# Kernel optimization log

Hardware: AMD Instinct MI355X
Metric: run time of the kernel (lower is better)

Reference implementation:

```python
import jax, jax.numpy as jnp
import numpy as np

NUM_HEADS = 16
D_KV = 64
NUM_BUCKETS = 32
MAX_DISTANCE = 128


def _relative_position_bucket(rel_pos, num_buckets=NUM_BUCKETS, max_distance=MAX_DISTANCE):
    # bidirectional bucketing (dec_or_not=False -> b_di=True in source)
    nb = num_buckets // 2
    buckets = (rel_pos > 0).astype(jnp.int32) * nb
    rel = jnp.abs(rel_pos)
    max_exact = nb // 2
    is_small = rel < max_exact
    # guard log(0); masked out by is_small anyway
    rel_if_large = max_exact + (
        jnp.log(jnp.maximum(rel, 1).astype(jnp.float32) / max_exact)
        / np.log(max_distance / max_exact) * (nb - max_exact)
    ).astype(jnp.int32)
    rel_if_large = jnp.minimum(rel_if_large, nb - 1)
    return buckets + jnp.where(is_small, rel, rel_if_large)


def setup_inputs() -> dict:
    key = jax.random.key(0)
    ks = jax.random.split(key, 6)
    B, S, D = 2, 2048, 1024
    s = 1.0 / np.sqrt(D)
    return {
        "hidden_states": jax.random.normal(ks[0], (B, S, D), jnp.float32),
        "Wq": jax.random.normal(ks[1], (D, NUM_HEADS * D_KV), jnp.float32) * s,
        "Wk": jax.random.normal(ks[2], (D, NUM_HEADS * D_KV), jnp.float32) * s,
        "Wv": jax.random.normal(ks[3], (D, NUM_HEADS * D_KV), jnp.float32) * s,
        "Wo": jax.random.normal(ks[4], (NUM_HEADS * D_KV, D), jnp.float32) * s,
        "rel_emb": jax.random.normal(ks[5], (NUM_BUCKETS, NUM_HEADS), jnp.float32),
    }


def reference(hidden_states, Wq, Wk, Wv, Wo, rel_emb):
    B, S, D = hidden_states.shape
    H, Dh = NUM_HEADS, D_KV

    def heads(x):  # [B,S,H*Dh] -> [B,H,S,Dh]
        return x.reshape(B, S, H, Dh).transpose(0, 2, 1, 3)

    q = heads(hidden_states @ Wq)
    k = heads(hidden_states @ Wk)
    v = heads(hidden_states @ Wv)

    # T5 attention: no 1/sqrt(d) scaling
    scores = jnp.einsum("bhqd,bhkd->bhqk", q, k)

    # relative position bias (bias_cal)
    pos = jnp.arange(S)
    rel_pos = pos[None, :] - pos[:, None]  # [S_q, S_k]
    buckets = _relative_position_bucket(rel_pos)
    bias = rel_emb[buckets]                       # [S,S,H]
    bias = bias.transpose(2, 0, 1)[None]          # [1,H,S,S]

    scores = scores + bias
    attn = jax.nn.softmax(scores.astype(jnp.float32), axis=-1).astype(scores.dtype)
    # dropout p=0 in eval -> identity
    out = jnp.einsum("bhqk,bhkd->bhqd", attn, v)
    out = out.transpose(0, 2, 1, 3).reshape(B, S, H * Dh)
    return out @ Wo
```

## Files before the change

kernel.cpp:

```cpp
#include <hip/hip_runtime.h>

typedef __bf16 bf16x8 __attribute__((ext_vector_type(8)));
typedef float f32x4 __attribute__((ext_vector_type(4)));

#define LDK 72
#define LOG2E 1.44269504088896f

__device__ __forceinline__ unsigned short bfbits(float x) {
  __bf16 h = (__bf16)x;
  return __builtin_bit_cast(unsigned short, h);
}

__global__ void bias_table_kernel(const float* __restrict__ rel_emb,
                                  float* __restrict__ tab) {
  int i = blockIdx.x * 256 + threadIdx.x;
  int h = i >> 12;
  int idx = i & 4095;
  int rp = idx - 2048;
  int base = (rp > 0) ? 16 : 0;
  int rel = rp < 0 ? -rp : rp;
  int b;
  if (rel < 8) {
    b = rel;
  } else {
    b = 8 + (int)(log2f((float)rel * 0.125f) * 2.0f);
    if (b > 15) b = 15;
  }
  tab[h * 4096 + idx] = rel_emb[(base + b) * 16 + h] * LOG2E;
}

__global__ __launch_bounds__(256)
void transpose_w_kernel(const float* __restrict__ W0, const float* __restrict__ W1,
                        const float* __restrict__ W2, const float* __restrict__ W3,
                        unsigned short* __restrict__ T0, unsigned short* __restrict__ T1,
                        unsigned short* __restrict__ T2, unsigned short* __restrict__ T3) {
  __shared__ __align__(16) unsigned short Tlds[64 * 68];
  const int mz = blockIdx.z;
  const float* W = mz == 0 ? W0 : (mz == 1 ? W1 : (mz == 2 ? W2 : W3));
  unsigned short* T = mz == 0 ? T0 : (mz == 1 ? T1 : (mz == 2 ? T2 : T3));
  const int k0 = blockIdx.y * 64, n0 = blockIdx.x * 64, tid = threadIdx.x;
#pragma unroll
  for (int p = 0; p < 4; ++p) {
    int idx = p * 256 + tid;
    int kk = idx >> 4, nc = idx & 15;
    float4 v = *(const float4*)(W + (size_t)(k0 + kk) * 1024 + n0 + nc * 4);
    ushort4 s;
    s.x = bfbits(v.x); s.y = bfbits(v.y); s.z = bfbits(v.z); s.w = bfbits(v.w);
    *(ushort4*)(Tlds + kk * 68 + nc * 4) = s;
  }
  __syncthreads();
#pragma unroll
  for (int p = 0; p < 2; ++p) {
    int idx = p * 256 + tid;
    int n = idx >> 3, c = idx & 7;
    unsigned short tmp[8];
#pragma unroll
    for (int j = 0; j < 8; ++j) tmp[j] = Tlds[(c * 8 + j) * 68 + n];
    *(uint4*)(T + (size_t)(n0 + n) * 1024 + k0 + c * 8) = *(const uint4*)tmp;
  }
}

template <bool A_F32, bool OUT_F32, int BN>
__global__ __launch_bounds__(256)
void gemm_kernel(const void* __restrict__ Av,
                 const unsigned short* __restrict__ Wt0,
                 const unsigned short* __restrict__ Wt1,
                 const unsigned short* __restrict__ Wt2,
                 void* __restrict__ O0v, void* __restrict__ O1v, void* __restrict__ O2v,
                 float scale0) {
  constexpr int NBLK = 1024 / BN;
  constexpr int NT = BN / 32;
  __shared__ __align__(16) unsigned short Alds[128 * LDK];
  __shared__ __align__(16) unsigned short Wlds[BN * LDK];
  const int tid = threadIdx.x;
  const int which = blockIdx.x / NBLK;
  const int n0 = (blockIdx.x % NBLK) * BN;
  const int m0 = blockIdx.y * 128;
  const unsigned short* Wt = which == 0 ? Wt0 : (which == 1 ? Wt1 : Wt2);
  void* Ov = which == 0 ? O0v : (which == 1 ? O1v : O2v);
  const int wave = tid >> 6, lane = tid & 63, quad = lane >> 4, col = lane & 15;
  const int wm = (wave >> 1) * 64, wn = (wave & 1) * (BN / 2);

  f32x4 acc[4][NT] = {};

  for (int kt = 0; kt < 16; ++kt) {
    const int k0 = kt * 64;
    __syncthreads();
    if (A_F32) {
      const float* A = (const float*)Av;
#pragma unroll
      for (int p = 0; p < 8; ++p) {
        int idx = p * 256 + tid;
        int m = idx >> 4, c = idx & 15;
        float4 v = *(const float4*)(A + (size_t)(m0 + m) * 1024 + k0 + c * 4);
        ushort4 s;
        s.x = bfbits(v.x); s.y = bfbits(v.y); s.z = bfbits(v.z); s.w = bfbits(v.w);
        *(ushort4*)(Alds + m * LDK + c * 4) = s;
      }
    } else {
      const unsigned short* A = (const unsigned short*)Av;
#pragma unroll
      for (int p = 0; p < 4; ++p) {
        int idx = p * 256 + tid;
        int m = idx >> 3, c = idx & 7;
        uint4 v = *(const uint4*)(A + (size_t)(m0 + m) * 1024 + k0 + c * 8);
        *(uint4*)(Alds + m * LDK + c * 8) = v;
      }
    }
#pragma unroll
    for (int p = 0; p < BN / 32; ++p) {
      int idx = p * 256 + tid;
      int n = idx >> 3, c = idx & 7;
      uint4 v = *(const uint4*)(Wt + (size_t)(n0 + n) * 1024 + k0 + c * 8);
      *(uint4*)(Wlds + n * LDK + c * 8) = v;
    }
    __syncthreads();
#pragma unroll
    for (int ks = 0; ks < 2; ++ks) {
      bf16x8 af[4], wf[NT];
#pragma unroll
      for (int mt = 0; mt < 4; ++mt)
        af[mt] = *(const bf16x8*)(Alds + (wm + mt * 16 + col) * LDK + ks * 32 + quad * 8);
#pragma unroll
      for (int nt = 0; nt < NT; ++nt)
        wf[nt] = *(const bf16x8*)(Wlds + (wn + nt * 16 + col) * LDK + ks * 32 + quad * 8);
#pragma unroll
      for (int mt = 0; mt < 4; ++mt)
#pragma unroll
        for (int nt = 0; nt < NT; ++nt)
          acc[mt][nt] = __builtin_amdgcn_mfma_f32_16x16x32_bf16(af[mt], wf[nt], acc[mt][nt], 0, 0, 0);
    }
  }
  if (!OUT_F32 && which == 2) {
    unsigned short* Ot = (unsigned short*)Ov;
#pragma unroll
    for (int nt = 0; nt < NT; ++nt)
#pragma unroll
      for (int mt = 0; mt < 4; ++mt) {
        int n = n0 + wn + nt * 16 + col;
        int m = m0 + wm + mt * 16 + quad * 4;
        ushort4 s;
        s.x = bfbits(acc[mt][nt][0]); s.y = bfbits(acc[mt][nt][1]);
        s.z = bfbits(acc[mt][nt][2]); s.w = bfbits(acc[mt][nt][3]);
        *(ushort4*)(Ot + (size_t)n * 4096 + m) = s;
      }
  } else {
    const float sc = (which == 0) ? scale0 : 1.0f;
#pragma unroll
    for (int mt = 0; mt < 4; ++mt)
#pragma unroll
      for (int nt = 0; nt < NT; ++nt)
#pragma unroll
        for (int r = 0; r < 4; ++r) {
          int m = m0 + wm + mt * 16 + quad * 4 + r;
          int n = n0 + wn + nt * 16 + col;
          float x = acc[mt][nt][r] * sc;
          if (OUT_F32)
            ((float*)Ov)[(size_t)m * 1024 + n] = x;
          else
            ((unsigned short*)Ov)[(size_t)m * 1024 + n] = bfbits(x);
        }
  }
}

__global__ __launch_bounds__(256)
void attn_kernel(unsigned short* __restrict__ q_ws,
                 const unsigned short* __restrict__ k_ws,
                 const unsigned short* __restrict__ vt_ws,
                 const float* __restrict__ bias_tab) {
  __shared__ __align__(16) unsigned short Klds[64 * LDK];
  __shared__ __align__(16) unsigned short Vlds[64 * LDK];
  __shared__ __align__(16) unsigned short Plds[128 * LDK];
  __shared__ float bias_lds[192];
  __shared__ float l_sh[128];
  const int tid = threadIdx.x;
  const int q0 = blockIdx.x * 128;
  const int bh = blockIdx.y;
  const int b = bh >> 4, h = bh & 15;
  const int wave = tid >> 6, lane = tid & 63, quad = lane >> 4, col = lane & 15;

  bf16x8 qf[2][2];
#pragma unroll
  for (int nt = 0; nt < 2; ++nt) {
    size_t row = (size_t)(b * 2048 + q0 + wave * 32 + nt * 16 + col) * 1024 + h * 64;
    qf[nt][0] = *(const bf16x8*)(q_ws + row + quad * 8);
    qf[nt][1] = *(const bf16x8*)(q_ws + row + 32 + quad * 8);
  }

  float l_lane[2] = {0.f, 0.f};
  f32x4 of[2][4] = {};

  for (int kt = 0; kt < 32; ++kt) {
    const int k0 = kt * 64;
    __syncthreads();
#pragma unroll
    for (int p = 0; p < 2; ++p) {
      int idx = p * 256 + tid;
      int key = idx >> 3, c = idx & 7;
      *(uint4*)(Klds + key * LDK + c * 8) =
          *(const uint4*)(k_ws + (size_t)(b * 2048 + k0 + key) * 1024 + h * 64 + c * 8);
    }
#pragma unroll
    for (int p = 0; p < 2; ++p) {
      int idx = p * 256 + tid;
      int d = idx >> 3, c = idx & 7;
      *(uint4*)(Vlds + d * LDK + c * 8) =
          *(const uint4*)(vt_ws + (size_t)(h * 64 + d) * 4096 + b * 2048 + k0 + c * 8);
    }
    if (tid < 191) bias_lds[tid] = bias_tab[h * 4096 + 2048 + k0 - q0 - 127 + tid];
    __syncthreads();

    f32x4 st[4][2];
#pragma unroll
    for (int mt = 0; mt < 4; ++mt)
#pragma unroll
      for (int nt = 0; nt < 2; ++nt)
#pragma unroll
        for (int r = 0; r < 4; ++r)
          st[mt][nt][r] =
              bias_lds[(mt * 16 + quad * 4 + r) - (wave * 32 + nt * 16 + col) + 127];
#pragma unroll
    for (int ks = 0; ks < 2; ++ks)
#pragma unroll
      for (int mt = 0; mt < 4; ++mt) {
        bf16x8 kf = *(const bf16x8*)(Klds + (mt * 16 + col) * LDK + ks * 32 + quad * 8);
        st[mt][0] = __builtin_amdgcn_mfma_f32_16x16x32_bf16(kf, qf[0][ks], st[mt][0], 0, 0, 0);
        st[mt][1] = __builtin_amdgcn_mfma_f32_16x16x32_bf16(kf, qf[1][ks], st[mt][1], 0, 0, 0);
      }

#pragma unroll
    for (int nt = 0; nt < 2; ++nt)
#pragma unroll
      for (int mt = 0; mt < 4; ++mt) {
        float p0 = __builtin_amdgcn_exp2f(st[mt][nt][0] - 64.f);
        float p1 = __builtin_amdgcn_exp2f(st[mt][nt][1] - 64.f);
        float p2 = __builtin_amdgcn_exp2f(st[mt][nt][2] - 64.f);
        float p3 = __builtin_amdgcn_exp2f(st[mt][nt][3] - 64.f);
        l_lane[nt] += (p0 + p1) + (p2 + p3);
        ushort4 pk;
        pk.x = bfbits(p0); pk.y = bfbits(p1); pk.z = bfbits(p2); pk.w = bfbits(p3);
        *(ushort4*)(Plds + (wave * 32 + nt * 16 + col) * LDK + mt * 16 + quad * 4) = pk;
      }
    __threadfence_block();

#pragma unroll
    for (int ks = 0; ks < 2; ++ks) {
      bf16x8 pf0 = *(const bf16x8*)(Plds + (wave * 32 + col) * LDK + ks * 32 + quad * 8);
      bf16x8 pf1 = *(const bf16x8*)(Plds + (wave * 32 + 16 + col) * LDK + ks * 32 + quad * 8);
#pragma unroll
      for (int dn = 0; dn < 4; ++dn) {
        bf16x8 vf = *(const bf16x8*)(Vlds + (dn * 16 + col) * LDK + ks * 32 + quad * 8);
        of[0][dn] = __builtin_amdgcn_mfma_f32_16x16x32_bf16(pf0, vf, of[0][dn], 0, 0, 0);
        of[1][dn] = __builtin_amdgcn_mfma_f32_16x16x32_bf16(pf1, vf, of[1][dn], 0, 0, 0);
      }
    }
  }

#pragma unroll
  for (int nt = 0; nt < 2; ++nt) {
    l_lane[nt] += __shfl_xor(l_lane[nt], 16, 64);
    l_lane[nt] += __shfl_xor(l_lane[nt], 32, 64);
  }
  l_sh[wave * 32 + col] = l_lane[0];
  l_sh[wave * 32 + 16 + col] = l_lane[1];
  __syncthreads();
#pragma unroll
  for (int mtp = 0; mtp < 2; ++mtp)
#pragma unroll
    for (int r = 0; r < 4; ++r) {
      float inv = 1.0f / fmaxf(l_sh[wave * 32 + mtp * 16 + quad * 4 + r], 1e-30f);
      size_t row = (size_t)(b * 2048 + q0 + wave * 32 + mtp * 16 + quad * 4 + r);
#pragma unroll
      for (int dn = 0; dn < 4; ++dn)
        q_ws[row * 1024 + h * 64 + dn * 16 + col] = bfbits(of[mtp][dn][r] * inv);
    }
}

extern "C" void kernel_launch(void* const* d_in, const int* in_sizes, int n_in,
                              void* d_out, int out_size, void* d_ws, size_t ws_size,
                              hipStream_t stream) {
  const float* hidden = (const float*)d_in[0];
  const float* Wq = (const float*)d_in[1];
  const float* Wk = (const float*)d_in[2];
  const float* Wv = (const float*)d_in[3];
  const float* Wo = (const float*)d_in[4];
  const float* rel_emb = (const float*)d_in[5];
  float* out = (float*)d_out;

  unsigned short* q_ws = (unsigned short*)d_ws;
  unsigned short* k_ws = q_ws + 4194304;
  unsigned short* vt_ws = k_ws + 4194304;
  unsigned short* wt_q = vt_ws + 4194304;
  unsigned short* wt_k = wt_q + 1048576;
  unsigned short* wt_v = wt_k + 1048576;
  unsigned short* wt_o = wt_v + 1048576;
  float* bias_tab = (float*)(wt_o + 1048576);

  bias_table_kernel<<<256, 256, 0, stream>>>(rel_emb, bias_tab);
  transpose_w_kernel<<<dim3(16, 16, 4), 256, 0, stream>>>(
      Wq, Wk, Wv, Wo, wt_q, wt_k, wt_v, wt_o);
  gemm_kernel<true, false, 128><<<dim3(24, 32), 256, 0, stream>>>(
      hidden, wt_q, wt_k, wt_v, q_ws, k_ws, vt_ws, LOG2E);
  attn_kernel<<<dim3(16, 32), 256, 0, stream>>>(q_ws, k_ws, vt_ws, bias_tab);
  gemm_kernel<false, true, 64><<<dim3(16, 32), 256, 0, stream>>>(
      q_ws, wt_o, wt_o, wt_o, out, out, out, 1.0f);
}
```

Before: 239.4 us.

## Split attention over key halves with merge pass; pre-convert hidden states to bf16

The attention kernel now splits the key range into two halves along a new grid dimension, doubling the block count from 512 to 1024 so more CUs are occupied. Each half writes unnormalized partial outputs and row sums to scratch, and a separate merge kernel adds them and normalizes. The merge is correct without max rescaling because the original kernel does not track a running max. Hidden states are also converted to bf16 once in a standalone kernel, so the QKV GEMM loads bf16 A tiles instead of converting fp32 in every block. The cost is extra global traffic for the partial outputs, two extra launches, and the partial sums being rounded to bf16.

```diff
diff --git a/kernel.cpp b/kernel.cpp
--- a/kernel.cpp
+++ b/kernel.cpp
@@ -30,6 +30,16 @@
 }
 
 __global__ __launch_bounds__(256)
+void hid_convert_kernel(const float* __restrict__ src, unsigned short* __restrict__ dst) {
+  int idx = (blockIdx.x * 256 + threadIdx.x) * 8;
+  float4 v0 = *(const float4*)(src + idx);
+  float4 v1 = *(const float4*)(src + idx + 4);
+  unsigned short o[8] = {bfbits(v0.x), bfbits(v0.y), bfbits(v0.z), bfbits(v0.w),
+                         bfbits(v1.x), bfbits(v1.y), bfbits(v1.z), bfbits(v1.w)};
+  *(uint4*)(dst + idx) = *(const uint4*)o;
+}
+
+__global__ __launch_bounds__(256)
 void transpose_w_kernel(const float* __restrict__ W0, const float* __restrict__ W1,
                         const float* __restrict__ W2, const float* __restrict__ W3,
                         unsigned short* __restrict__ T0, unsigned short* __restrict__ T1,
@@ -60,9 +70,9 @@
   }
 }
 
-template <bool A_F32, bool OUT_F32, int BN>
-__global__ __launch_bounds__(256)
-void gemm_kernel(const void* __restrict__ Av,
+template <bool OUT_F32, int BN>
+__global__ __launch_bounds__(256)
+void gemm_kernel(const unsigned short* __restrict__ A,
                  const unsigned short* __restrict__ Wt0,
                  const unsigned short* __restrict__ Wt1,
                  const unsigned short* __restrict__ Wt2,
@@ -86,26 +96,12 @@
   for (int kt = 0; kt < 16; ++kt) {
     const int k0 = kt * 64;
     __syncthreads();
-    if (A_F32) {
-      const float* A = (const float*)Av;
-#pragma unroll
-      for (int p = 0; p < 8; ++p) {
-        int idx = p * 256 + tid;
-        int m = idx >> 4, c = idx & 15;
-        float4 v = *(const float4*)(A + (size_t)(m0 + m) * 1024 + k0 + c * 4);
-        ushort4 s;
-        s.x = bfbits(v.x); s.y = bfbits(v.y); s.z = bfbits(v.z); s.w = bfbits(v.w);
-        *(ushort4*)(Alds + m * LDK + c * 4) = s;
-      }
-    } else {
-      const unsigned short* A = (const unsigned short*)Av;
-#pragma unroll
-      for (int p = 0; p < 4; ++p) {
-        int idx = p * 256 + tid;
-        int m = idx >> 3, c = idx & 7;
-        uint4 v = *(const uint4*)(A + (size_t)(m0 + m) * 1024 + k0 + c * 8);
-        *(uint4*)(Alds + m * LDK + c * 8) = v;
-      }
+#pragma unroll
+    for (int p = 0; p < 4; ++p) {
+      int idx = p * 256 + tid;
+      int m = idx >> 3, c = idx & 7;
+      uint4 v = *(const uint4*)(A + (size_t)(m0 + m) * 1024 + k0 + c * 8);
+      *(uint4*)(Alds + m * LDK + c * 8) = v;
     }
 #pragma unroll
     for (int p = 0; p < BN / 32; ++p) {
@@ -164,19 +160,21 @@
 }
 
 __global__ __launch_bounds__(256)
-void attn_kernel(unsigned short* __restrict__ q_ws,
+void attn_kernel(const unsigned short* __restrict__ q_ws,
                  const unsigned short* __restrict__ k_ws,
                  const unsigned short* __restrict__ vt_ws,
-                 const float* __restrict__ bias_tab) {
+                 const float* __restrict__ bias_tab,
+                 unsigned short* __restrict__ pO,
+                 float* __restrict__ l_ws) {
   __shared__ __align__(16) unsigned short Klds[64 * LDK];
   __shared__ __align__(16) unsigned short Vlds[64 * LDK];
   __shared__ __align__(16) unsigned short Plds[128 * LDK];
   __shared__ float bias_lds[192];
-  __shared__ float l_sh[128];
   const int tid = threadIdx.x;
   const int q0 = blockIdx.x * 128;
   const int bh = blockIdx.y;
   const int b = bh >> 4, h = bh & 15;
+  const int split = blockIdx.z;
   const int wave = tid >> 6, lane = tid & 63, quad = lane >> 4, col = lane & 15;
 
   bf16x8 qf[2][2];
@@ -190,7 +188,7 @@
   float l_lane[2] = {0.f, 0.f};
   f32x4 of[2][4] = {};
 
-  for (int kt = 0; kt < 32; ++kt) {
+  for (int kt = split * 16; kt < split * 16 + 16; ++kt) {
     const int k0 = kt * 64;
     __syncthreads();
 #pragma unroll
@@ -256,24 +254,43 @@
     }
   }
 
+  unsigned short* pOs = pO + (size_t)split * 4194304;
 #pragma unroll
   for (int nt = 0; nt < 2; ++nt) {
     l_lane[nt] += __shfl_xor(l_lane[nt], 16, 64);
     l_lane[nt] += __shfl_xor(l_lane[nt], 32, 64);
-  }
-  l_sh[wave * 32 + col] = l_lane[0];
-  l_sh[wave * 32 + 16 + col] = l_lane[1];
-  __syncthreads();
+    if (quad == 0)
+      l_ws[(size_t)split * 65536 + (b * 2048 + q0 + wave * 32 + nt * 16 + col) * 16 + h] =
+          l_lane[nt];
+  }
 #pragma unroll
   for (int mtp = 0; mtp < 2; ++mtp)
 #pragma unroll
     for (int r = 0; r < 4; ++r) {
-      float inv = 1.0f / fmaxf(l_sh[wave * 32 + mtp * 16 + quad * 4 + r], 1e-30f);
       size_t row = (size_t)(b * 2048 + q0 + wave * 32 + mtp * 16 + quad * 4 + r);
 #pragma unroll
       for (int dn = 0; dn < 4; ++dn)
-        q_ws[row * 1024 + h * 64 + dn * 16 + col] = bfbits(of[mtp][dn][r] * inv);
-    }
+        pOs[row * 1024 + h * 64 + dn * 16 + col] = bfbits(of[mtp][dn][r]);
+    }
+}
+
+__global__ __launch_bounds__(256)
+void merge_kernel(const unsigned short* __restrict__ pO,
+                  const float* __restrict__ l_ws,
+                  unsigned short* __restrict__ q_ws) {
+  int idx = (blockIdx.x * 256 + threadIdx.x) * 8;
+  int token = idx >> 10;
+  int h = (idx & 1023) >> 6;
+  float l0 = l_ws[token * 16 + h];
+  float l1 = l_ws[65536 + token * 16 + h];
+  float inv = 1.0f / fmaxf(l0 + l1, 1e-35f);
+  bf16x8 a = *(const bf16x8*)(pO + idx);
+  bf16x8 c = *(const bf16x8*)(pO + 4194304 + idx);
+  unsigned short o[8];
+#pragma unroll
+  for (int j = 0; j < 8; ++j)
+    o[j] = bfbits(((float)a[j] + (float)c[j]) * inv);
+  *(uint4*)(q_ws + idx) = *(const uint4*)o;
 }
 
 extern "C" void kernel_launch(void* const* d_in, const int* in_sizes, int n_in,
@@ -295,13 +312,18 @@
   unsigned short* wt_v = wt_k + 1048576;
   unsigned short* wt_o = wt_v + 1048576;
   float* bias_tab = (float*)(wt_o + 1048576);
+  unsigned short* scratch = (unsigned short*)d_out;
+  float* l_ws = (float*)wt_q;
 
   bias_table_kernel<<<256, 256, 0, stream>>>(rel_emb, bias_tab);
+  hid_convert_kernel<<<2048, 256, 0, stream>>>(hidden, scratch);
   transpose_w_kernel<<<dim3(16, 16, 4), 256, 0, stream>>>(
       Wq, Wk, Wv, Wo, wt_q, wt_k, wt_v, wt_o);
-  gemm_kernel<true, false, 128><<<dim3(24, 32), 256, 0, stream>>>(
-      hidden, wt_q, wt_k, wt_v, q_ws, k_ws, vt_ws, LOG2E);
-  attn_kernel<<<dim3(16, 32), 256, 0, stream>>>(q_ws, k_ws, vt_ws, bias_tab);
-  gemm_kernel<false, true, 64><<<dim3(16, 32), 256, 0, stream>>>(
+  gemm_kernel<false, 128><<<dim3(24, 32), 256, 0, stream>>>(
+      scratch, wt_q, wt_k, wt_v, q_ws, k_ws, vt_ws, LOG2E);
+  attn_kernel<<<dim3(16, 32, 2), 256, 0, stream>>>(
+      q_ws, k_ws, vt_ws, bias_tab, scratch, l_ws);
+  merge_kernel<<<2048, 256, 0, stream>>>(scratch, l_ws, q_ws);
+  gemm_kernel<true, 64><<<dim3(16, 32), 256, 0, stream>>>(
       q_ws, wt_o, wt_o, wt_o, out, out, out, 1.0f);
 }
```

Result: slower. 244.7 us (+2.2%).

## Use direct global-to-LDS loads in GEMM, pre-convert hidden to bf16, constant far bias

Applied to the files above, without the earlier changes.

Adds a kernel that converts hidden states to bf16 once, using the output buffer as scratch. The GEMM becomes bf16-only and stages tiles with global_load_lds straight into unpadded shared memory, removing register round-trips. The attention kernel treats key tiles beyond the max distance as a constant bias and skips the per-tile bias load. Risks include LDS bank conflicts from the removed padding and an extra kernel launch.

```diff
diff --git a/kernel.cpp b/kernel.cpp
--- a/kernel.cpp
+++ b/kernel.cpp
@@ -9,6 +9,12 @@
 __device__ __forceinline__ unsigned short bfbits(float x) {
   __bf16 h = (__bf16)x;
   return __builtin_bit_cast(unsigned short, h);
+}
+
+__device__ __forceinline__ void gload_lds16(const unsigned short* g, unsigned short* l) {
+  __builtin_amdgcn_global_load_lds(
+      (const __attribute__((address_space(1))) unsigned int*)(const void*)g,
+      (__attribute__((address_space(3))) unsigned int*)(void*)l, 16, 0, 0);
 }
 
 __global__ void bias_table_kernel(const float* __restrict__ rel_emb,
@@ -30,6 +36,16 @@
 }
 
 __global__ __launch_bounds__(256)
+void hid_convert_kernel(const float* __restrict__ src, unsigned short* __restrict__ dst) {
+  int idx = (blockIdx.x * 256 + threadIdx.x) * 8;
+  float4 v0 = *(const float4*)(src + idx);
+  float4 v1 = *(const float4*)(src + idx + 4);
+  unsigned short o[8] = {bfbits(v0.x), bfbits(v0.y), bfbits(v0.z), bfbits(v0.w),
+                         bfbits(v1.x), bfbits(v1.y), bfbits(v1.z), bfbits(v1.w)};
+  *(uint4*)(dst + idx) = *(const uint4*)o;
+}
+
+__global__ __launch_bounds__(256)
 void transpose_w_kernel(const float* __restrict__ W0, const float* __restrict__ W1,
                         const float* __restrict__ W2, const float* __restrict__ W3,
                         unsigned short* __restrict__ T0, unsigned short* __restrict__ T1,
@@ -60,9 +76,9 @@
   }
 }
 
-template <bool A_F32, bool OUT_F32, int BN>
+template <bool OUT_F32, int BN>
 __global__ __launch_bounds__(256)
-void gemm_kernel(const void* __restrict__ Av,
+void gemm_kernel(const unsigned short* __restrict__ A,
                  const unsigned short* __restrict__ Wt0,
                  const unsigned short* __restrict__ Wt1,
                  const unsigned short* __restrict__ Wt2,
@@ -70,8 +86,8 @@
                  float scale0) {
   constexpr int NBLK = 1024 / BN;
   constexpr int NT = BN / 32;
-  __shared__ __align__(16) unsigned short Alds[128 * LDK];
-  __shared__ __align__(16) unsigned short Wlds[BN * LDK];
+  __shared__ __align__(16) unsigned short Alds[128 * 64];
+  __shared__ __align__(16) unsigned short Wlds[BN * 64];
   const int tid = threadIdx.x;
   const int which = blockIdx.x / NBLK;
   const int n0 = (blockIdx.x % NBLK) * BN;
@@ -80,39 +96,26 @@
   void* Ov = which == 0 ? O0v : (which == 1 ? O1v : O2v);
   const int wave = tid >> 6, lane = tid & 63, quad = lane >> 4, col = lane & 15;
   const int wm = (wave >> 1) * 64, wn = (wave & 1) * (BN / 2);
+  const int wbase = tid & ~63;
 
   f32x4 acc[4][NT] = {};
 
   for (int kt = 0; kt < 16; ++kt) {
     const int k0 = kt * 64;
     __syncthreads();
-    if (A_F32) {
-      const float* A = (const float*)Av;
-#pragma unroll
-      for (int p = 0; p < 8; ++p) {
-        int idx = p * 256 + tid;
-        int m = idx >> 4, c = idx & 15;
-        float4 v = *(const float4*)(A + (size_t)(m0 + m) * 1024 + k0 + c * 4);
-        ushort4 s;
-        s.x = bfbits(v.x); s.y = bfbits(v.y); s.z = bfbits(v.z); s.w = bfbits(v.w);
-        *(ushort4*)(Alds + m * LDK + c * 4) = s;
-      }
-    } else {
-      const unsigned short* A = (const unsigned short*)Av;
-#pragma unroll
-      for (int p = 0; p < 4; ++p) {
-        int idx = p * 256 + tid;
-        int m = idx >> 3, c = idx & 7;
-        uint4 v = *(const uint4*)(A + (size_t)(m0 + m) * 1024 + k0 + c * 8);
-        *(uint4*)(Alds + m * LDK + c * 8) = v;
-      }
+#pragma unroll
+    for (int p = 0; p < 4; ++p) {
+      int idx = p * 256 + tid;
+      int m = idx >> 3, c = idx & 7;
+      gload_lds16(A + (size_t)(m0 + m) * 1024 + k0 + c * 8,
+                  Alds + (size_t)(p * 256 + wbase) * 8);
     }
 #pragma unroll
     for (int p = 0; p < BN / 32; ++p) {
       int idx = p * 256 + tid;
       int n = idx >> 3, c = idx & 7;
-      uint4 v = *(const uint4*)(Wt + (size_t)(n0 + n) * 1024 + k0 + c * 8);
-      *(uint4*)(Wlds + n * LDK + c * 8) = v;
+      gload_lds16(Wt + (size_t)(n0 + n) * 1024 + k0 + c * 8,
+                  Wlds + (size_t)(p * 256 + wbase) * 8);
     }
     __syncthreads();
 #pragma unroll
@@ -120,10 +123,10 @@
       bf16x8 af[4], wf[NT];
 #pragma unroll
       for (int mt = 0; mt < 4; ++mt)
-        af[mt] = *(const bf16x8*)(Alds + (wm + mt * 16 + col) * LDK + ks * 32 + quad * 8);
+        af[mt] = *(const bf16x8*)(Alds + (wm + mt * 16 + col) * 64 + ks * 32 + quad * 8);
 #pragma unroll
       for (int nt = 0; nt < NT; ++nt)
-        wf[nt] = *(const bf16x8*)(Wlds + (wn + nt * 16 + col) * LDK + ks * 32 + quad * 8);
+        wf[nt] = *(const bf16x8*)(Wlds + (wn + nt * 16 + col) * 64 + ks * 32 + quad * 8);
 #pragma unroll
       for (int mt = 0; mt < 4; ++mt)
 #pragma unroll
@@ -186,12 +189,16 @@
     qf[nt][0] = *(const bf16x8*)(q_ws + row + quad * 8);
     qf[nt][1] = *(const bf16x8*)(q_ws + row + 32 + quad * 8);
   }
+  const float bias_far_pos = bias_tab[h * 4096 + 2048 + 512];
+  const float bias_far_neg = bias_tab[h * 4096 + 2048 - 512];
 
   float l_lane[2] = {0.f, 0.f};
   f32x4 of[2][4] = {};
 
   for (int kt = 0; kt < 32; ++kt) {
     const int k0 = kt * 64;
+    const int diff = k0 - q0;
+    const bool far = (diff >= 256) || (diff <= -192);
     __syncthreads();
 #pragma unroll
     for (int p = 0; p < 2; ++p) {
@@ -207,18 +214,29 @@
       *(uint4*)(Vlds + d * LDK + c * 8) =
           *(const uint4*)(vt_ws + (size_t)(h * 64 + d) * 4096 + b * 2048 + k0 + c * 8);
     }
-    if (tid < 191) bias_lds[tid] = bias_tab[h * 4096 + 2048 + k0 - q0 - 127 + tid];
+    if (!far && tid < 191)
+      bias_lds[tid] = bias_tab[h * 4096 + 2048 + k0 - q0 - 127 + tid];
     __syncthreads();
 
     f32x4 st[4][2];
-#pragma unroll
-    for (int mt = 0; mt < 4; ++mt)
-#pragma unroll
-      for (int nt = 0; nt < 2; ++nt)
-#pragma unroll
-        for (int r = 0; r < 4; ++r)
-          st[mt][nt][r] =
-              bias_lds[(mt * 16 + quad * 4 + r) - (wave * 32 + nt * 16 + col) + 127];
+    if (far) {
+      const float c0 = (diff > 0) ? bias_far_pos : bias_far_neg;
+#pragma unroll
+      for (int mt = 0; mt < 4; ++mt)
+#pragma unroll
+        for (int nt = 0; nt < 2; ++nt)
+#pragma unroll
+          for (int r = 0; r < 4; ++r) st[mt][nt][r] = c0;
+    } else {
+#pragma unroll
+      for (int mt = 0; mt < 4; ++mt)
+#pragma unroll
+        for (int nt = 0; nt < 2; ++nt)
+#pragma unroll
+          for (int r = 0; r < 4; ++r)
+            st[mt][nt][r] =
+                bias_lds[(mt * 16 + quad * 4 + r) - (wave * 32 + nt * 16 + col) + 127];
+    }
 #pragma unroll
     for (int ks = 0; ks < 2; ++ks)
 #pragma unroll
@@ -295,13 +313,15 @@
   unsigned short* wt_v = wt_k + 1048576;
   unsigned short* wt_o = wt_v + 1048576;
   float* bias_tab = (float*)(wt_o + 1048576);
+  unsigned short* hid_bf = (unsigned short*)d_out;
 
   bias_table_kernel<<<256, 256, 0, stream>>>(rel_emb, bias_tab);
+  hid_convert_kernel<<<2048, 256, 0, stream>>>(hidden, hid_bf);
   transpose_w_kernel<<<dim3(16, 16, 4), 256, 0, stream>>>(
       Wq, Wk, Wv, Wo, wt_q, wt_k, wt_v, wt_o);
-  gemm_kernel<true, false, 128><<<dim3(24, 32), 256, 0, stream>>>(
-      hidden, wt_q, wt_k, wt_v, q_ws, k_ws, vt_ws, LOG2E);
+  gemm_kernel<false, 128><<<dim3(24, 32), 256, 0, stream>>>(
+      hid_bf, wt_q, wt_k, wt_v, q_ws, k_ws, vt_ws, LOG2E);
   attn_kernel<<<dim3(16, 32), 256, 0, stream>>>(q_ws, k_ws, vt_ws, bias_tab);
-  gemm_kernel<false, true, 64><<<dim3(16, 32), 256, 0, stream>>>(
+  gemm_kernel<true, 64><<<dim3(16, 32), 256, 0, stream>>>(
       q_ws, wt_o, wt_o, wt_o, out, out, out, 1.0f);
 }
```

Measured after the change: 221.1 us. -7.7%, faster.
